# Performance work log

Hardware: AMD Instinct MI355X
Metric: run time of the kernel (lower is better)

Reference implementation:

```python
import jax, jax.numpy as jnp
import numpy as np

N, D, E, H, K = 8192, 1024, 8, 256, 2


def setup_inputs() -> dict:
    key = jax.random.key(0)
    ks = jax.random.split(key, 9)
    s = 0.02
    return {
        "x": jax.random.normal(ks[0], (N, D), dtype=jnp.float32),
        "Wg": jax.random.normal(ks[1], (D, E), dtype=jnp.float32) * s,
        "bg": jnp.zeros((E,), dtype=jnp.float32),
        "W1": jax.random.normal(ks[2], (E, D, H), dtype=jnp.float32) * s,
        "b1": jnp.zeros((E, H), dtype=jnp.float32),
        "W2": jax.random.normal(ks[3], (E, H, H), dtype=jnp.float32) * s,
        "b2": jnp.zeros((E, H), dtype=jnp.float32),
        "W3": jax.random.normal(ks[4], (E, H, D), dtype=jnp.float32) * s,
        "b3": jnp.zeros((E, D), dtype=jnp.float32),
    }


def reference(x, Wg, bg, W1, b1, W2, b2, W3, b3):
    # Gating: softmax over experts, then keep only top-k gate values per token.
    gates = jax.nn.softmax(x @ Wg + bg, axis=-1)              # [N, E]
    top_v, top_i = jax.lax.top_k(gates, K)                    # [N, K]
    rows = jnp.arange(gates.shape[0])[:, None]                # [N, 1]
    top_k_gates = jnp.zeros_like(gates).at[rows, top_i].set(top_v)  # [N, E]

    # Dense all-expert MLP (matches original: every expert runs on every token).
    h = jax.nn.relu(jnp.einsum('nd,edh->neh', x, W1) + b1)    # [N, E, H]
    h = jax.nn.relu(jnp.einsum('neh,ehg->neg', h, W2) + b2)   # [N, E, H]  (dropout is eval no-op)
    eo = jax.nn.relu(jnp.einsum('neh,ehd->ned', h, W3) + b3)  # [N, E, D]

    # Combine with masked gates: einsum('...nde,...ne->...nd') with eo in 'ned' layout.
    output = jnp.einsum('ned,ne->nd', eo, top_k_gates)        # [N, D]
    return output
```

## Files before the change

### kernel.cpp

```cpp
#include <hip/hip_runtime.h>
#include <math.h>

#define NTOK 8192
#define DDIM 1024
#define NEXP 8
#define HDIM 256
#define TOPK 2
#define PADM 128
#define CAPS (NTOK * TOPK + NEXP * PADM)
#define NT64  (CAPS / 64)
#define NT128 (CAPS / 128)

typedef __attribute__((ext_vector_type(8))) __bf16 bf16x8;
typedef __attribute__((ext_vector_type(4))) float f32x4;

#define GLDS16(g, s)                                                      \
    __builtin_amdgcn_global_load_lds(                                     \
        (const __attribute__((address_space(1))) void*)(g),               \
        (__attribute__((address_space(3))) void*)(s), 16, 0, 0)

static constexpr size_t OFF_TOFF = 128;
static constexpr size_t OFF_ZBUF = 4096;
static constexpr size_t OFF_T2E  = 8192;
static constexpr size_t OFF_T2G  = OFF_T2E + (size_t)NTOK * TOPK * 4;
static constexpr size_t OFF_SLOT = OFF_T2G + (size_t)NTOK * TOPK * 4;
static constexpr size_t OFF_TOK  = OFF_SLOT + (size_t)NTOK * TOPK * 4;
static constexpr size_t OFF_GAT  = OFF_TOK + (size_t)CAPS * 4;
static constexpr size_t OFF_XB   = (OFF_GAT + (size_t)CAPS * 4 + 255) & ~(size_t)255;
static constexpr size_t OFF_W1T  = OFF_XB  + (size_t)NTOK * DDIM * 2;
static constexpr size_t OFF_W2T  = OFF_W1T + (size_t)NEXP * DDIM * HDIM * 2;
static constexpr size_t OFF_W3T  = OFF_W2T + (size_t)NEXP * HDIM * HDIM * 2;
static constexpr size_t OFF_H2   = OFF_W3T + (size_t)NEXP * HDIM * DDIM * 2;
static constexpr size_t OFF_H3   = OFF_H2  + (size_t)CAPS * HDIM * 2;

static __device__ __forceinline__ unsigned short f2b(float f) {
    __bf16 h = (__bf16)f;
    return __builtin_bit_cast(unsigned short, h);
}
static __device__ __forceinline__ float b2f(unsigned short u) {
    return __builtin_bit_cast(float, ((unsigned)u) << 16);
}

__global__ __launch_bounds__(256) void gate_trans(
    const float* __restrict__ x, const float* __restrict__ Wg,
    const float* __restrict__ bg, unsigned short* __restrict__ xb,
    int* __restrict__ top2e, float* __restrict__ top2g,
    const float* __restrict__ W1, const float* __restrict__ W2,
    const float* __restrict__ W3, __bf16* __restrict__ w1t,
    __bf16* __restrict__ w2t, __bf16* __restrict__ w3t)
{
    __shared__ __align__(16) float sh[NEXP * DDIM];
    const int tid = threadIdx.x;

    if (blockIdx.x < 256) {
        for (int d = tid; d < DDIM; d += 256) {
            const float4 w0 = *(const float4*)(Wg + (size_t)d * NEXP);
            const float4 w1 = *(const float4*)(Wg + (size_t)d * NEXP + 4);
            sh[0 * DDIM + d] = w0.x; sh[1 * DDIM + d] = w0.y;
            sh[2 * DDIM + d] = w0.z; sh[3 * DDIM + d] = w0.w;
            sh[4 * DDIM + d] = w1.x; sh[5 * DDIM + d] = w1.y;
            sh[6 * DDIM + d] = w1.z; sh[7 * DDIM + d] = w1.w;
        }
        __syncthreads();

        const int n = (blockIdx.y * 256 + blockIdx.x) * 4 + (tid >> 6);
        const int lane = tid & 63;
        const float* xr = x + (size_t)n * DDIM;
        unsigned short* xbr = xb + (size_t)n * DDIM;

        float acc[NEXP];
#pragma unroll
        for (int e = 0; e < NEXP; ++e) acc[e] = 0.f;

#pragma unroll
        for (int it = 0; it < 4; ++it) {
            const int d = it * 256 + lane * 4;
            const float4 xv = *(const float4*)(xr + d);
            ushort4 u;
            u.x = f2b(xv.x); u.y = f2b(xv.y); u.z = f2b(xv.z); u.w = f2b(xv.w);
            *(ushort4*)(xbr + d) = u;
#pragma unroll
            for (int e = 0; e < NEXP; ++e) {
                const float4 wt = *(const float4*)(sh + e * DDIM + d);
                acc[e] = fmaf(xv.x, wt.x, acc[e]);
                acc[e] = fmaf(xv.y, wt.y, acc[e]);
                acc[e] = fmaf(xv.z, wt.z, acc[e]);
                acc[e] = fmaf(xv.w, wt.w, acc[e]);
            }
        }
#pragma unroll
        for (int off = 32; off > 0; off >>= 1)
#pragma unroll
            for (int e = 0; e < NEXP; ++e) acc[e] += __shfl_down(acc[e], off, 64);

        if (lane == 0) {
            float v[NEXP], mx = -1e30f;
#pragma unroll
            for (int e = 0; e < NEXP; ++e) { v[e] = acc[e] + bg[e]; mx = fmaxf(mx, v[e]); }
            float p[NEXP], s = 0.f;
#pragma unroll
            for (int e = 0; e < NEXP; ++e) { p[e] = expf(v[e] - mx); s += p[e]; }
            const float inv = 1.f / s;
#pragma unroll
            for (int e = 0; e < NEXP; ++e) p[e] *= inv;
            int i0 = 0;
#pragma unroll
            for (int e = 1; e < NEXP; ++e) if (p[e] > p[i0]) i0 = e;
            int i1 = (i0 == 0) ? 1 : 0;
#pragma unroll
            for (int e = 0; e < NEXP; ++e) if (e != i0 && p[e] > p[i1]) i1 = e;
            top2e[n * 2 + 0] = i0;  top2e[n * 2 + 1] = i1;
            top2g[n * 2 + 0] = p[i0]; top2g[n * 2 + 1] = p[i1];
        }
    } else {
        const int e = blockIdx.y;
        int bt = blockIdx.x - 256;
        const float* Wi; __bf16* Wo; int R, C, xt, yt;
        if (bt < 256)      { Wi = W1; Wo = w1t; R = DDIM; C = HDIM; xt = bt & 7;  yt = bt >> 3; }
        else if (bt < 320) { bt -= 256; Wi = W2; Wo = w2t; R = HDIM; C = HDIM; xt = bt & 7;  yt = bt >> 3; }
        else               { bt -= 320; Wi = W3; Wo = w3t; R = HDIM; C = DDIM; xt = bt & 31; yt = bt >> 5; }
        const int r0 = yt * 32, c0 = xt * 32;
        const int tx = tid & 31, ty = tid >> 5;
        const float* Wie = Wi + (size_t)e * R * C;
        __bf16* Woe = Wo + (size_t)e * C * R;
#pragma unroll
        for (int j = 0; j < 4; ++j)
            sh[(ty + j * 8) * 33 + tx] = Wie[(size_t)(r0 + ty + j * 8) * C + c0 + tx];
        __syncthreads();
#pragma unroll
        for (int j = 0; j < 4; ++j)
            Woe[(size_t)(c0 + ty + j * 8) * R + r0 + tx] = (__bf16)sh[tx * 33 + ty + j * 8];
    }
}

__global__ __launch_bounds__(1024) void route(
    const int* __restrict__ top2e, const float* __restrict__ top2g,
    int* __restrict__ toff, int* __restrict__ tok, float* __restrict__ gat,
    int* __restrict__ slotof, float* __restrict__ zbuf)
{
    const int tid = threadIdx.x;
    const int wv = tid >> 6, ln = tid & 63;
    __shared__ int   waveTot[16][NEXP];
    __shared__ int   waveBase[16][NEXP];
    __shared__ int   totS[NEXP];
    __shared__ int   toffS[NEXP + 1];
    __shared__ short excS[1024][NEXP];

    zbuf[tid] = 0.f;

    int myE[16]; float myG[16];
    const int4*   pe = (const int4*)(top2e + tid * 16);
    const float4* pg = (const float4*)(top2g + tid * 16);
#pragma unroll
    for (int q = 0; q < 4; ++q) {
        const int4 v = pe[q];
        myE[q * 4 + 0] = v.x; myE[q * 4 + 1] = v.y;
        myE[q * 4 + 2] = v.z; myE[q * 4 + 3] = v.w;
        const float4 g = pg[q];
        myG[q * 4 + 0] = g.x; myG[q * 4 + 1] = g.y;
        myG[q * 4 + 2] = g.z; myG[q * 4 + 3] = g.w;
    }

#pragma unroll
    for (int e = 0; e < NEXP; ++e) {
        int c = 0;
#pragma unroll
        for (int j = 0; j < 16; ++j) c += (myE[j] == e);
        int inc = c;
#pragma unroll
        for (int off = 1; off < 64; off <<= 1) {
            const int t = __shfl_up(inc, off, 64);
            if (ln >= off) inc += t;
        }
        excS[tid][e] = (short)(inc - c);
        if (ln == 63) waveTot[wv][e] = inc;
    }
    __syncthreads();

    if (tid < NEXP) {
        int b = 0;
#pragma unroll
        for (int w = 0; w < 16; ++w) {
            const int t = waveTot[w][tid];
            waveBase[w][tid] = b;
            b += t;
        }
        totS[tid] = b;
    }
    __syncthreads();

    if (tid == 0) {
        int acc = 0;
#pragma unroll
        for (int e = 0; e < NEXP; ++e) {
            toffS[e] = acc;
            acc += (totS[e] + PADM - 1) & ~(PADM - 1);
        }
        toffS[NEXP] = acc;
#pragma unroll
        for (int e = 0; e <= NEXP; ++e) toff[e] = toffS[e];
    }
    __syncthreads();

#pragma unroll
    for (int j = 0; j < 16; ++j) {
        int pre = 0;
#pragma unroll
        for (int j2 = 0; j2 < j; ++j2) pre += (myE[j2] == myE[j]);
        const int e = myE[j];
        const int slot = toffS[e] + waveBase[wv][e] + (int)excS[tid][e] + pre;
        const int i = tid * 16 + j;
        tok[slot] = i >> 1;
        gat[slot] = myG[j];
        slotof[i] = slot;
    }

#pragma unroll
    for (int e = 0; e < NEXP; ++e) {
        const int begin = toffS[e] + totS[e];
        const int end   = toffS[e + 1];
        for (int i = begin + tid; i < end; i += 1024) {
            tok[i] = -1;
            gat[i] = 0.f;
        }
    }
}

__global__ __launch_bounds__(256) void egemm12(
    const __bf16* __restrict__ xb, const __bf16* __restrict__ w1t,
    const __bf16* __restrict__ w2t, const float* __restrict__ b1,
    const float* __restrict__ b2, const int* __restrict__ toff,
    const int* __restrict__ tok, const char* __restrict__ zbuf,
    __bf16* __restrict__ h2)
{
    const int total = toff[NEXP];
    const int slot0 = blockIdx.x * 64;
    if (slot0 >= total) return;
    int e = 0;
    while (toff[e + 1] <= slot0) ++e;

    __shared__ __align__(16) char smem[73728];
    char* AsB = smem;
    char* BsB = smem + 8192;
    char* H1s = smem + 40960;

    const int tid  = threadIdx.x;
    const int lane = tid & 63;
    const int wid  = tid >> 6;

    const int srow  = tid >> 3;
    const int sslot = tid & 7;
    const int ks    = sslot ^ (srow & 7);

    const __bf16* We1 = w1t + (size_t)e * HDIM * DDIM;
    const char* ap[2];
#pragma unroll
    for (int i = 0; i < 2; ++i) {
        const int t = tok[slot0 + i * 32 + srow];
        ap[i] = (t >= 0) ? (const char*)(xb + (size_t)t * DDIM + ks * 8) : zbuf;
    }
    const char* bp1[8];
#pragma unroll
    for (int i = 0; i < 8; ++i)
        bp1[i] = (const char*)(We1 + (size_t)(i * 32 + srow) * DDIM + ks * 8);

    const int llo = lane & 15, lhi = lane >> 4;
    const int m7 = llo & 7;
    int abyte[4], bbyte[4];
#pragma unroll
    for (int m = 0; m < 4; ++m) {
        abyte[m] = (m * 16 + llo) * 128;
        bbyte[m] = (wid * 64 + m * 16 + llo) * 128;
    }

    f32x4 acc[4][4];
#pragma unroll
    for (int m = 0; m < 4; ++m)
#pragma unroll
        for (int n = 0; n < 4; ++n) acc[m][n] = (f32x4){0.f, 0.f, 0.f, 0.f};

    for (int k0 = 0; k0 < DDIM; k0 += 64) {
        const size_t kb = (size_t)k0 * 2;
        GLDS16(ap[0] + kb, AsB + tid * 16);
        GLDS16(ap[1] + kb, AsB + 4096 + tid * 16);
#pragma unroll
        for (int i = 0; i < 8; ++i)
            GLDS16(bp1[i] + kb, BsB + i * 4096 + tid * 16);
        __syncthreads();
#pragma unroll
        for (int kk = 0; kk < 2; ++kk) {
            const int sl = ((kk << 2) + lhi) ^ m7;
            bf16x8 af[4], bfr[4];
#pragma unroll
            for (int m = 0; m < 4; ++m) af[m]  = *(const bf16x8*)(AsB + abyte[m] + (sl << 4));
#pragma unroll
            for (int n = 0; n < 4; ++n) bfr[n] = *(const bf16x8*)(BsB + bbyte[n] + (sl << 4));
#pragma unroll
            for (int m = 0; m < 4; ++m)
#pragma unroll
                for (int n = 0; n < 4; ++n)
                    acc[m][n] = __builtin_amdgcn_mfma_f32_16x16x32_bf16(
                        af[m], bfr[n], acc[m][n], 0, 0, 0);
        }
        __syncthreads();
    }

    {
        const float* be1 = b1 + (size_t)e * HDIM;
#pragma unroll
        for (int n = 0; n < 4; ++n) {
            const int col = wid * 64 + n * 16 + llo;
            const float bb = be1[col];
            const int colbyte = (col & 7) * 2;
            const int slice = col >> 3;
#pragma unroll
            for (int m = 0; m < 4; ++m) {
#pragma unroll
                for (int j = 0; j < 4; ++j) {
                    const int r = m * 16 + lhi * 4 + j;
                    const float v = fmaxf(acc[m][n][j] + bb, 0.f);
                    *(__bf16*)(H1s + r * 512 + ((slice ^ (r & 7)) << 4) + colbyte) = (__bf16)v;
                }
                acc[m][n] = (f32x4){0.f, 0.f, 0.f, 0.f};
            }
        }
    }
    __syncthreads();

    const __bf16* We2 = w2t + (size_t)e * HDIM * HDIM;
    const char* bp2[8];
#pragma unroll
    for (int i = 0; i < 8; ++i)
        bp2[i] = (const char*)(We2 + (size_t)(i * 32 + srow) * HDIM + ks * 8);

    for (int k2 = 0; k2 < 4; ++k2) {
        const size_t kb = (size_t)k2 * 128;
#pragma unroll
        for (int i = 0; i < 8; ++i)
            GLDS16(bp2[i] + kb, BsB + i * 4096 + tid * 16);
        __syncthreads();
#pragma unroll
        for (int kk = 0; kk < 2; ++kk) {
            const int slB = ((kk << 2) + lhi) ^ m7;
            const int sA  = k2 * 8 + (kk << 2) + lhi;
            const int slA = sA ^ m7;
            bf16x8 af[4], bfr[4];
#pragma unroll
            for (int m = 0; m < 4; ++m)
                af[m] = *(const bf16x8*)(H1s + (m * 16 + llo) * 512 + (slA << 4));
#pragma unroll
            for (int n = 0; n < 4; ++n)
                bfr[n] = *(const bf16x8*)(BsB + bbyte[n] + (slB << 4));
#pragma unroll
            for (int m = 0; m < 4; ++m)
#pragma unroll
                for (int n = 0; n < 4; ++n)
                    acc[m][n] = __builtin_amdgcn_mfma_f32_16x16x32_bf16(
                        af[m], bfr[n], acc[m][n], 0, 0, 0);
        }
        __syncthreads();
    }

    {
        const float* be2 = b2 + (size_t)e * HDIM;
#pragma unroll
        for (int n = 0; n < 4; ++n) {
            const int col = wid * 64 + n * 16 + llo;
            const float bb = be2[col];
#pragma unroll
            for (int m = 0; m < 4; ++m) {
#pragma unroll
                for (int j = 0; j < 4; ++j) {
                    const int r = slot0 + m * 16 + lhi * 4 + j;
                    h2[(size_t)r * HDIM + col] = (__bf16)fmaxf(acc[m][n][j] + bb, 0.f);
                }
            }
        }
    }
}

template<int KDIM, int NCOL>
__global__ __launch_bounds__(256) void egemm3(
    const __bf16* __restrict__ Ain, const __bf16* __restrict__ Wt,
    const float* __restrict__ ball, const int* __restrict__ toff,
    const float* __restrict__ gat, __bf16* __restrict__ Out)
{
    const int total = toff[NEXP];
    const int slot0 = blockIdx.y * 128;
    if (slot0 >= total) return;
    int e = 0;
    while (toff[e + 1] <= slot0) ++e;
    const int col0 = blockIdx.x * 128;

    __shared__ __align__(16) char smem[32768];
    char* AsB = smem;
    char* BsB = smem + 16384;

    const int tid  = threadIdx.x;
    const int lane = tid & 63;
    const int wid  = tid >> 6;
    const int wr = wid >> 1, wc = wid & 1;

    const int srow  = tid >> 3;
    const int sslot = tid & 7;
    const int ks    = sslot ^ (srow & 7);
    const __bf16* We = Wt + (size_t)e * NCOL * KDIM;
    const char* ap[4];
    const char* bp[4];
#pragma unroll
    for (int i = 0; i < 4; ++i) {
        const int row = i * 32 + srow;
        ap[i] = (const char*)(Ain + (size_t)(slot0 + row) * KDIM + ks * 8);
        bp[i] = (const char*)(We + (size_t)(col0 + row) * KDIM + ks * 8);
    }

    const int llo = lane & 15, lhi = lane >> 4;
    const int m7 = llo & 7;
    int abyte[4], bbyte[4];
#pragma unroll
    for (int m = 0; m < 4; ++m) {
        abyte[m] = (wr * 64 + m * 16 + llo) * 128;
        bbyte[m] = (wc * 64 + m * 16 + llo) * 128;
    }

    f32x4 acc[4][4];
#pragma unroll
    for (int m = 0; m < 4; ++m)
#pragma unroll
        for (int n = 0; n < 4; ++n) acc[m][n] = (f32x4){0.f, 0.f, 0.f, 0.f};

    for (int k0 = 0; k0 < KDIM; k0 += 64) {
        const size_t kb = (size_t)k0 * 2;
#pragma unroll
        for (int i = 0; i < 4; ++i)
            GLDS16(ap[i] + kb, AsB + i * 4096 + wid * 1024);
#pragma unroll
        for (int i = 0; i < 4; ++i)
            GLDS16(bp[i] + kb, BsB + i * 4096 + wid * 1024);
        __syncthreads();
#pragma unroll
        for (int kk = 0; kk < 2; ++kk) {
            const int sl = ((kk << 2) + lhi) ^ m7;
            bf16x8 af[4], bfr[4];
#pragma unroll
            for (int m = 0; m < 4; ++m) af[m]  = *(const bf16x8*)(AsB + abyte[m] + (sl << 4));
#pragma unroll
            for (int n = 0; n < 4; ++n) bfr[n] = *(const bf16x8*)(BsB + bbyte[n] + (sl << 4));
#pragma unroll
            for (int m = 0; m < 4; ++m)
#pragma unroll
                for (int n = 0; n < 4; ++n)
                    acc[m][n] = __builtin_amdgcn_mfma_f32_16x16x32_bf16(
                        af[m], bfr[n], acc[m][n], 0, 0, 0);
        }
        __syncthreads();
    }

    const float* be = ball + (size_t)e * NCOL;
#pragma unroll
    for (int m = 0; m < 4; ++m) {
        const int rbase = slot0 + wr * 64 + m * 16 + lhi * 4;
        float g[4];
#pragma unroll
        for (int j = 0; j < 4; ++j) g[j] = gat[rbase + j];
#pragma unroll
        for (int n = 0; n < 4; ++n) {
            const int col = col0 + wc * 64 + n * 16 + llo;
            const float bb = be[col];
#pragma unroll
            for (int j = 0; j < 4; ++j) {
                const float v = fmaxf(acc[m][n][j] + bb, 0.f) * g[j];
                Out[(size_t)(rbase + j) * NCOL + col] = (__bf16)v;
            }
        }
    }
}

__global__ __launch_bounds__(256) void combine(
    const unsigned short* __restrict__ h3, const int* __restrict__ slotof,
    float* __restrict__ out)
{
    const int n = blockIdx.x;
    const int c = threadIdx.x * 4;
    const int s0 = slotof[n * 2], s1 = slotof[n * 2 + 1];
    const ushort4 a = *(const ushort4*)(h3 + (size_t)s0 * DDIM + c);
    const ushort4 b = *(const ushort4*)(h3 + (size_t)s1 * DDIM + c);
    float4 o;
    o.x = b2f(a.x) + b2f(b.x);
    o.y = b2f(a.y) + b2f(b.y);
    o.z = b2f(a.z) + b2f(b.z);
    o.w = b2f(a.w) + b2f(b.w);
    *(float4*)(out + (size_t)n * DDIM + c) = o;
}

extern "C" void kernel_launch(void* const* d_in, const int* in_sizes, int n_in,
                              void* d_out, int out_size, void* d_ws, size_t ws_size,
                              hipStream_t stream)
{
    const float* x  = (const float*)d_in[0];
    const float* Wg = (const float*)d_in[1];
    const float* bg = (const float*)d_in[2];
    const float* W1 = (const float*)d_in[3];
    const float* b1 = (const float*)d_in[4];
    const float* W2 = (const float*)d_in[5];
    const float* b2 = (const float*)d_in[6];
    const float* W3 = (const float*)d_in[7];
    const float* b3 = (const float*)d_in[8];
    float* out = (float*)d_out;

    char* ws = (char*)d_ws;
    int*   toff   = (int*)(ws + OFF_TOFF);
    char*  zbuf   = ws + OFF_ZBUF;
    int*   top2e  = (int*)(ws + OFF_T2E);
    float* top2g  = (float*)(ws + OFF_T2G);
    int*   slotof = (int*)(ws + OFF_SLOT);
    int*   tok    = (int*)(ws + OFF_TOK);
    float* gat    = (float*)(ws + OFF_GAT);
    unsigned short* xbu = (unsigned short*)(ws + OFF_XB);
    __bf16* xb  = (__bf16*)(ws + OFF_XB);
    __bf16* w1t = (__bf16*)(ws + OFF_W1T);
    __bf16* w2t = (__bf16*)(ws + OFF_W2T);
    __bf16* w3t = (__bf16*)(ws + OFF_W3T);
    __bf16* h2  = (__bf16*)(ws + OFF_H2);
    __bf16* h3  = (__bf16*)(ws + OFF_H3);

    gate_trans<<<dim3(832, NEXP), 256, 0, stream>>>(
        x, Wg, bg, xbu, top2e, top2g, W1, W2, W3, w1t, w2t, w3t);
    route<<<1, 1024, 0, stream>>>(top2e, top2g, toff, tok, gat, slotof, (float*)zbuf);

    egemm12<<<NT64, 256, 0, stream>>>(xb, w1t, w2t, b1, b2, toff, tok, zbuf, h2);
    egemm3<HDIM, DDIM><<<dim3(DDIM / 128, NT128), 256, 0, stream>>>(
        h2, w3t, b3, toff, gat, h3);

    combine<<<NTOK, 256, 0, stream>>>((const unsigned short*)h3, slotof, out);
}
```

Baseline: 106.8 us.

## Fuse all MoE stages into one persistent cooperative kernel with grid syncs

Replaces the five separate launches (gate/transpose, route, expert GEMM1+2, GEMM3, combine) with one persistent cooperative kernel. Stages are separated by grid.sync, and work is distributed with grid-stride loops over a grid sized from occupancy. Routing now runs in a single 256-thread block instead of 1024 threads. The goal is to remove launch gaps and inter-kernel drain. In exchange, occupancy is capped at about two blocks per CU by a 72KB LDS allocation, and grid barriers plus the serial routing stage add latency.

```diff
diff --git a/kernel.cpp b/kernel.cpp
--- a/kernel.cpp
+++ b/kernel.cpp
@@ -1,5 +1,8 @@
 #include <hip/hip_runtime.h>
+#include <hip/hip_cooperative_groups.h>
 #include <math.h>
+
+namespace cg = cooperative_groups;
 
 #define NTOK 8192
 #define DDIM 1024
@@ -8,8 +11,6 @@
 #define TOPK 2
 #define PADM 128
 #define CAPS (NTOK * TOPK + NEXP * PADM)
-#define NT64  (CAPS / 64)
-#define NT128 (CAPS / 128)
 
 typedef __attribute__((ext_vector_type(8))) __bf16 bf16x8;
 typedef __attribute__((ext_vector_type(4))) float f32x4;
@@ -41,456 +42,461 @@
     return __builtin_bit_cast(float, ((unsigned)u) << 16);
 }
 
-__global__ __launch_bounds__(256) void gate_trans(
-    const float* __restrict__ x, const float* __restrict__ Wg,
-    const float* __restrict__ bg, unsigned short* __restrict__ xb,
-    int* __restrict__ top2e, float* __restrict__ top2g,
-    const float* __restrict__ W1, const float* __restrict__ W2,
-    const float* __restrict__ W3, __bf16* __restrict__ w1t,
-    __bf16* __restrict__ w2t, __bf16* __restrict__ w3t)
+__global__ __launch_bounds__(256, 2) void moe_mega(
+    const float* __restrict__ x,  const float* __restrict__ Wg,
+    const float* __restrict__ bg, const float* __restrict__ W1,
+    const float* __restrict__ b1, const float* __restrict__ W2,
+    const float* __restrict__ b2, const float* __restrict__ W3,
+    const float* __restrict__ b3, float* __restrict__ out,
+    char* __restrict__ ws)
 {
-    __shared__ __align__(16) float sh[NEXP * DDIM];
+    cg::grid_group grid = cg::this_grid();
+    __shared__ __align__(16) char smem[73728];
+
+    int*   toff   = (int*)(ws + OFF_TOFF);
+    float* zbuf   = (float*)(ws + OFF_ZBUF);
+    int*   top2e  = (int*)(ws + OFF_T2E);
+    float* top2g  = (float*)(ws + OFF_T2G);
+    int*   slotof = (int*)(ws + OFF_SLOT);
+    int*   tok    = (int*)(ws + OFF_TOK);
+    float* gat    = (float*)(ws + OFF_GAT);
+    unsigned short* xbu = (unsigned short*)(ws + OFF_XB);
+    __bf16* xb  = (__bf16*)(ws + OFF_XB);
+    __bf16* w1t = (__bf16*)(ws + OFF_W1T);
+    __bf16* w2t = (__bf16*)(ws + OFF_W2T);
+    __bf16* w3t = (__bf16*)(ws + OFF_W3T);
+    __bf16* h2  = (__bf16*)(ws + OFF_H2);
+    __bf16* h3  = (__bf16*)(ws + OFF_H3);
+
     const int tid = threadIdx.x;
-
-    if (blockIdx.x < 256) {
+    const int bid = blockIdx.x;
+    const int nb  = gridDim.x;
+
+    {
+        float* WgT = (float*)smem;
         for (int d = tid; d < DDIM; d += 256) {
             const float4 w0 = *(const float4*)(Wg + (size_t)d * NEXP);
             const float4 w1 = *(const float4*)(Wg + (size_t)d * NEXP + 4);
-            sh[0 * DDIM + d] = w0.x; sh[1 * DDIM + d] = w0.y;
-            sh[2 * DDIM + d] = w0.z; sh[3 * DDIM + d] = w0.w;
-            sh[4 * DDIM + d] = w1.x; sh[5 * DDIM + d] = w1.y;
-            sh[6 * DDIM + d] = w1.z; sh[7 * DDIM + d] = w1.w;
+            WgT[0 * DDIM + d] = w0.x; WgT[1 * DDIM + d] = w0.y;
+            WgT[2 * DDIM + d] = w0.z; WgT[3 * DDIM + d] = w0.w;
+            WgT[4 * DDIM + d] = w1.x; WgT[5 * DDIM + d] = w1.y;
+            WgT[6 * DDIM + d] = w1.z; WgT[7 * DDIM + d] = w1.w;
         }
         __syncthreads();
 
-        const int n = (blockIdx.y * 256 + blockIdx.x) * 4 + (tid >> 6);
         const int lane = tid & 63;
-        const float* xr = x + (size_t)n * DDIM;
-        unsigned short* xbr = xb + (size_t)n * DDIM;
-
-        float acc[NEXP];
-#pragma unroll
-        for (int e = 0; e < NEXP; ++e) acc[e] = 0.f;
-
-#pragma unroll
-        for (int it = 0; it < 4; ++it) {
-            const int d = it * 256 + lane * 4;
-            const float4 xv = *(const float4*)(xr + d);
-            ushort4 u;
-            u.x = f2b(xv.x); u.y = f2b(xv.y); u.z = f2b(xv.z); u.w = f2b(xv.w);
-            *(ushort4*)(xbr + d) = u;
+        for (int g = bid; g < NTOK / 4; g += nb) {
+            const int n = g * 4 + (tid >> 6);
+            const float* xr = x + (size_t)n * DDIM;
+            unsigned short* xbr = xbu + (size_t)n * DDIM;
+
+            float acc[NEXP];
+#pragma unroll
+            for (int e = 0; e < NEXP; ++e) acc[e] = 0.f;
+#pragma unroll
+            for (int it = 0; it < 4; ++it) {
+                const int d = it * 256 + lane * 4;
+                const float4 xv = *(const float4*)(xr + d);
+                ushort4 u;
+                u.x = f2b(xv.x); u.y = f2b(xv.y); u.z = f2b(xv.z); u.w = f2b(xv.w);
+                *(ushort4*)(xbr + d) = u;
+#pragma unroll
+                for (int e = 0; e < NEXP; ++e) {
+                    const float4 wt = *(const float4*)(WgT + e * DDIM + d);
+                    acc[e] = fmaf(xv.x, wt.x, acc[e]);
+                    acc[e] = fmaf(xv.y, wt.y, acc[e]);
+                    acc[e] = fmaf(xv.z, wt.z, acc[e]);
+                    acc[e] = fmaf(xv.w, wt.w, acc[e]);
+                }
+            }
+#pragma unroll
+            for (int off = 32; off > 0; off >>= 1)
+#pragma unroll
+                for (int e = 0; e < NEXP; ++e) acc[e] += __shfl_down(acc[e], off, 64);
+
+            if (lane == 0) {
+                float v[NEXP], mx = -1e30f;
+#pragma unroll
+                for (int e = 0; e < NEXP; ++e) { v[e] = acc[e] + bg[e]; mx = fmaxf(mx, v[e]); }
+                float p[NEXP], s = 0.f;
+#pragma unroll
+                for (int e = 0; e < NEXP; ++e) { p[e] = expf(v[e] - mx); s += p[e]; }
+                const float inv = 1.f / s;
+#pragma unroll
+                for (int e = 0; e < NEXP; ++e) p[e] *= inv;
+                int i0 = 0;
+#pragma unroll
+                for (int e = 1; e < NEXP; ++e) if (p[e] > p[i0]) i0 = e;
+                int i1 = (i0 == 0) ? 1 : 0;
+#pragma unroll
+                for (int e = 0; e < NEXP; ++e) if (e != i0 && p[e] > p[i1]) i1 = e;
+                top2e[n * 2 + 0] = i0;  top2e[n * 2 + 1] = i1;
+                top2g[n * 2 + 0] = p[i0]; top2g[n * 2 + 1] = p[i1];
+            }
+        }
+
+        float* ts = (float*)(smem + 32768);
+        const int tx = tid & 31, ty = tid >> 5;
+        for (int t = bid; t < 4608; t += nb) {
+            const int e = t / 576;
+            int bt = t - e * 576;
+            const float* Wi; __bf16* Wo; int R, C, xt, yt;
+            if (bt < 256)      { Wi = W1; Wo = w1t; R = DDIM; C = HDIM; xt = bt & 7;  yt = bt >> 3; }
+            else if (bt < 320) { bt -= 256; Wi = W2; Wo = w2t; R = HDIM; C = HDIM; xt = bt & 7;  yt = bt >> 3; }
+            else               { bt -= 320; Wi = W3; Wo = w3t; R = HDIM; C = DDIM; xt = bt & 31; yt = bt >> 5; }
+            const int r0 = yt * 32, c0 = xt * 32;
+            const float* Wie = Wi + (size_t)e * R * C;
+            __bf16* Woe = Wo + (size_t)e * C * R;
+            __syncthreads();
+#pragma unroll
+            for (int j = 0; j < 4; ++j)
+                ts[(ty + j * 8) * 33 + tx] = Wie[(size_t)(r0 + ty + j * 8) * C + c0 + tx];
+            __syncthreads();
+#pragma unroll
+            for (int j = 0; j < 4; ++j)
+                Woe[(size_t)(c0 + ty + j * 8) * R + r0 + tx] = (__bf16)ts[tx * 33 + ty + j * 8];
+        }
+    }
+    grid.sync();
+
+    if (bid == 0) {
+        int* waveTotS  = (int*)smem;
+        int* waveBaseS = (int*)(smem + 128);
+        int* totS      = (int*)(smem + 256);
+        int* toffS     = (int*)(smem + 320);
+        const int wv = tid >> 6, ln = tid & 63;
+        const int4*   pe = (const int4*)top2e + tid * 16;
+        const float4* pg = (const float4*)top2g + tid * 16;
+
+        int c[NEXP] = {0, 0, 0, 0, 0, 0, 0, 0};
+        for (int q = 0; q < 16; ++q) {
+            const int4 v = pe[q];
+#pragma unroll
+            for (int e = 0; e < NEXP; ++e)
+                c[e] += (v.x == e) + (v.y == e) + (v.z == e) + (v.w == e);
+        }
+        int base[NEXP];
+#pragma unroll
+        for (int e = 0; e < NEXP; ++e) {
+            int inc = c[e];
+#pragma unroll
+            for (int off = 1; off < 64; off <<= 1) {
+                const int t = __shfl_up(inc, off, 64);
+                if (ln >= off) inc += t;
+            }
+            base[e] = inc - c[e];
+            if (ln == 63) waveTotS[wv * NEXP + e] = inc;
+        }
+        __syncthreads();
+        if (tid < NEXP) {
+            int b = 0;
+#pragma unroll
+            for (int w = 0; w < 4; ++w) {
+                const int t = waveTotS[w * NEXP + tid];
+                waveBaseS[w * NEXP + tid] = b;
+                b += t;
+            }
+            totS[tid] = b;
+        }
+        __syncthreads();
+        if (tid == 0) {
+            int acc = 0;
 #pragma unroll
             for (int e = 0; e < NEXP; ++e) {
-                const float4 wt = *(const float4*)(sh + e * DDIM + d);
-                acc[e] = fmaf(xv.x, wt.x, acc[e]);
-                acc[e] = fmaf(xv.y, wt.y, acc[e]);
-                acc[e] = fmaf(xv.z, wt.z, acc[e]);
-                acc[e] = fmaf(xv.w, wt.w, acc[e]);
-            }
-        }
-#pragma unroll
-        for (int off = 32; off > 0; off >>= 1)
-#pragma unroll
-            for (int e = 0; e < NEXP; ++e) acc[e] += __shfl_down(acc[e], off, 64);
-
-        if (lane == 0) {
-            float v[NEXP], mx = -1e30f;
-#pragma unroll
-            for (int e = 0; e < NEXP; ++e) { v[e] = acc[e] + bg[e]; mx = fmaxf(mx, v[e]); }
-            float p[NEXP], s = 0.f;
-#pragma unroll
-            for (int e = 0; e < NEXP; ++e) { p[e] = expf(v[e] - mx); s += p[e]; }
-            const float inv = 1.f / s;
-#pragma unroll
-            for (int e = 0; e < NEXP; ++e) p[e] *= inv;
-            int i0 = 0;
-#pragma unroll
-            for (int e = 1; e < NEXP; ++e) if (p[e] > p[i0]) i0 = e;
-            int i1 = (i0 == 0) ? 1 : 0;
-#pragma unroll
-            for (int e = 0; e < NEXP; ++e) if (e != i0 && p[e] > p[i1]) i1 = e;
-            top2e[n * 2 + 0] = i0;  top2e[n * 2 + 1] = i1;
-            top2g[n * 2 + 0] = p[i0]; top2g[n * 2 + 1] = p[i1];
-        }
-    } else {
-        const int e = blockIdx.y;
-        int bt = blockIdx.x - 256;
-        const float* Wi; __bf16* Wo; int R, C, xt, yt;
-        if (bt < 256)      { Wi = W1; Wo = w1t; R = DDIM; C = HDIM; xt = bt & 7;  yt = bt >> 3; }
-        else if (bt < 320) { bt -= 256; Wi = W2; Wo = w2t; R = HDIM; C = HDIM; xt = bt & 7;  yt = bt >> 3; }
-        else               { bt -= 320; Wi = W3; Wo = w3t; R = HDIM; C = DDIM; xt = bt & 31; yt = bt >> 5; }
-        const int r0 = yt * 32, c0 = xt * 32;
-        const int tx = tid & 31, ty = tid >> 5;
-        const float* Wie = Wi + (size_t)e * R * C;
-        __bf16* Woe = Wo + (size_t)e * C * R;
-#pragma unroll
-        for (int j = 0; j < 4; ++j)
-            sh[(ty + j * 8) * 33 + tx] = Wie[(size_t)(r0 + ty + j * 8) * C + c0 + tx];
+                toffS[e] = acc;
+                acc += (totS[e] + PADM - 1) & ~(PADM - 1);
+            }
+            toffS[NEXP] = acc;
+#pragma unroll
+            for (int e = 0; e <= NEXP; ++e) toff[e] = toffS[e];
+        }
         __syncthreads();
-#pragma unroll
-        for (int j = 0; j < 4; ++j)
-            Woe[(size_t)(c0 + ty + j * 8) * R + r0 + tx] = (__bf16)sh[tx * 33 + ty + j * 8];
+
+        int cur[NEXP];
+#pragma unroll
+        for (int e = 0; e < NEXP; ++e)
+            cur[e] = toffS[e] + waveBaseS[wv * NEXP + e] + base[e];
+
+        for (int q = 0; q < 16; ++q) {
+            const int4 v = pe[q];
+            const float4 gv = pg[q];
+            const int va[4] = {v.x, v.y, v.z, v.w};
+            const float ga[4] = {gv.x, gv.y, gv.z, gv.w};
+#pragma unroll
+            for (int j = 0; j < 4; ++j) {
+                int slot = 0;
+#pragma unroll
+                for (int e = 0; e < NEXP; ++e)
+                    if (va[j] == e) { slot = cur[e]; cur[e] = slot + 1; }
+                const int i = tid * 64 + q * 4 + j;
+                tok[slot] = i >> 1;
+                gat[slot] = ga[j];
+                slotof[i] = slot;
+            }
+        }
+#pragma unroll
+        for (int e = 0; e < NEXP; ++e)
+            for (int i = toffS[e] + totS[e] + tid; i < toffS[e + 1]; i += 256) {
+                tok[i] = -1;
+                gat[i] = 0.f;
+            }
+        for (int i = tid; i < 1024; i += 256) zbuf[i] = 0.f;
+        __threadfence();
     }
-}
-
-__global__ __launch_bounds__(1024) void route(
-    const int* __restrict__ top2e, const float* __restrict__ top2g,
-    int* __restrict__ toff, int* __restrict__ tok, float* __restrict__ gat,
-    int* __restrict__ slotof, float* __restrict__ zbuf)
-{
-    const int tid = threadIdx.x;
-    const int wv = tid >> 6, ln = tid & 63;
-    __shared__ int   waveTot[16][NEXP];
-    __shared__ int   waveBase[16][NEXP];
-    __shared__ int   totS[NEXP];
-    __shared__ int   toffS[NEXP + 1];
-    __shared__ short excS[1024][NEXP];
-
-    zbuf[tid] = 0.f;
-
-    int myE[16]; float myG[16];
-    const int4*   pe = (const int4*)(top2e + tid * 16);
-    const float4* pg = (const float4*)(top2g + tid * 16);
-#pragma unroll
-    for (int q = 0; q < 4; ++q) {
-        const int4 v = pe[q];
-        myE[q * 4 + 0] = v.x; myE[q * 4 + 1] = v.y;
-        myE[q * 4 + 2] = v.z; myE[q * 4 + 3] = v.w;
-        const float4 g = pg[q];
-        myG[q * 4 + 0] = g.x; myG[q * 4 + 1] = g.y;
-        myG[q * 4 + 2] = g.z; myG[q * 4 + 3] = g.w;
+    grid.sync();
+
+    {
+        const int total = toff[NEXP];
+        char* AsB = smem;
+        char* BsB = smem + 8192;
+        char* H1s = smem + 40960;
+        const int lane = tid & 63;
+        const int wid  = tid >> 6;
+        const int srow  = tid >> 3;
+        const int sslot = tid & 7;
+        const int ks    = sslot ^ (srow & 7);
+        const int llo = lane & 15, lhi = lane >> 4;
+        const int m7 = llo & 7;
+        int abyte[4], bbyte[4];
+#pragma unroll
+        for (int m = 0; m < 4; ++m) {
+            abyte[m] = (m * 16 + llo) * 128;
+            bbyte[m] = (wid * 64 + m * 16 + llo) * 128;
+        }
+
+        for (int t = bid; t < total / 64; t += nb) {
+            const int slot0 = t * 64;
+            int e = 0;
+            while (toff[e + 1] <= slot0) ++e;
+            __syncthreads();
+
+            const __bf16* We1 = w1t + (size_t)e * HDIM * DDIM;
+            const char* ap[2];
+#pragma unroll
+            for (int i = 0; i < 2; ++i) {
+                const int tk = tok[slot0 + i * 32 + srow];
+                ap[i] = (tk >= 0) ? (const char*)(xb + (size_t)tk * DDIM + ks * 8)
+                                  : (const char*)zbuf;
+            }
+            const char* bp1[8];
+#pragma unroll
+            for (int i = 0; i < 8; ++i)
+                bp1[i] = (const char*)(We1 + (size_t)(i * 32 + srow) * DDIM + ks * 8);
+
+            f32x4 acc[4][4];
+#pragma unroll
+            for (int m = 0; m < 4; ++m)
+#pragma unroll
+                for (int n = 0; n < 4; ++n) acc[m][n] = (f32x4){0.f, 0.f, 0.f, 0.f};
+
+            for (int k0 = 0; k0 < DDIM; k0 += 64) {
+                const size_t kb = (size_t)k0 * 2;
+                GLDS16(ap[0] + kb, AsB + tid * 16);
+                GLDS16(ap[1] + kb, AsB + 4096 + tid * 16);
+#pragma unroll
+                for (int i = 0; i < 8; ++i)
+                    GLDS16(bp1[i] + kb, BsB + i * 4096 + tid * 16);
+                __syncthreads();
+#pragma unroll
+                for (int kk = 0; kk < 2; ++kk) {
+                    const int sl = ((kk << 2) + lhi) ^ m7;
+                    bf16x8 af[4], bfr[4];
+#pragma unroll
+                    for (int m = 0; m < 4; ++m) af[m]  = *(const bf16x8*)(AsB + abyte[m] + (sl << 4));
+#pragma unroll
+                    for (int n = 0; n < 4; ++n) bfr[n] = *(const bf16x8*)(BsB + bbyte[n] + (sl << 4));
+#pragma unroll
+                    for (int m = 0; m < 4; ++m)
+#pragma unroll
+                        for (int n = 0; n < 4; ++n)
+                            acc[m][n] = __builtin_amdgcn_mfma_f32_16x16x32_bf16(
+                                af[m], bfr[n], acc[m][n], 0, 0, 0);
+                }
+                __syncthreads();
+            }
+
+            {
+                const float* be1 = b1 + (size_t)e * HDIM;
+#pragma unroll
+                for (int n = 0; n < 4; ++n) {
+                    const int col = wid * 64 + n * 16 + llo;
+                    const float bb = be1[col];
+                    const int colbyte = (col & 7) * 2;
+                    const int slice = col >> 3;
+#pragma unroll
+                    for (int m = 0; m < 4; ++m) {
+#pragma unroll
+                        for (int j = 0; j < 4; ++j) {
+                            const int r = m * 16 + lhi * 4 + j;
+                            const float v = fmaxf(acc[m][n][j] + bb, 0.f);
+                            *(__bf16*)(H1s + r * 512 + ((slice ^ (r & 7)) << 4) + colbyte) = (__bf16)v;
+                        }
+                        acc[m][n] = (f32x4){0.f, 0.f, 0.f, 0.f};
+                    }
+                }
+            }
+            __syncthreads();
+
+            const __bf16* We2 = w2t + (size_t)e * HDIM * HDIM;
+            const char* bp2[8];
+#pragma unroll
+            for (int i = 0; i < 8; ++i)
+                bp2[i] = (const char*)(We2 + (size_t)(i * 32 + srow) * HDIM + ks * 8);
+
+            for (int k2 = 0; k2 < 4; ++k2) {
+                const size_t kb = (size_t)k2 * 128;
+#pragma unroll
+                for (int i = 0; i < 8; ++i)
+                    GLDS16(bp2[i] + kb, BsB + i * 4096 + tid * 16);
+                __syncthreads();
+#pragma unroll
+                for (int kk = 0; kk < 2; ++kk) {
+                    const int slB = ((kk << 2) + lhi) ^ m7;
+                    const int sA  = k2 * 8 + (kk << 2) + lhi;
+                    const int slA = sA ^ m7;
+                    bf16x8 af[4], bfr[4];
+#pragma unroll
+                    for (int m = 0; m < 4; ++m)
+                        af[m] = *(const bf16x8*)(H1s + (m * 16 + llo) * 512 + (slA << 4));
+#pragma unroll
+                    for (int n = 0; n < 4; ++n)
+                        bfr[n] = *(const bf16x8*)(BsB + bbyte[n] + (slB << 4));
+#pragma unroll
+                    for (int m = 0; m < 4; ++m)
+#pragma unroll
+                        for (int n = 0; n < 4; ++n)
+                            acc[m][n] = __builtin_amdgcn_mfma_f32_16x16x32_bf16(
+                                af[m], bfr[n], acc[m][n], 0, 0, 0);
+                }
+                __syncthreads();
+            }
+
+            {
+                const float* be2 = b2 + (size_t)e * HDIM;
+#pragma unroll
+                for (int n = 0; n < 4; ++n) {
+                    const int col = wid * 64 + n * 16 + llo;
+                    const float bb = be2[col];
+#pragma unroll
+                    for (int m = 0; m < 4; ++m)
+#pragma unroll
+                        for (int j = 0; j < 4; ++j) {
+                            const int r = slot0 + m * 16 + lhi * 4 + j;
+                            h2[(size_t)r * HDIM + col] = (__bf16)fmaxf(acc[m][n][j] + bb, 0.f);
+                        }
+                }
+            }
+        }
     }
-
-#pragma unroll
-    for (int e = 0; e < NEXP; ++e) {
-        int c = 0;
-#pragma unroll
-        for (int j = 0; j < 16; ++j) c += (myE[j] == e);
-        int inc = c;
-#pragma unroll
-        for (int off = 1; off < 64; off <<= 1) {
-            const int t = __shfl_up(inc, off, 64);
-            if (ln >= off) inc += t;
-        }
-        excS[tid][e] = (short)(inc - c);
-        if (ln == 63) waveTot[wv][e] = inc;
+    grid.sync();
+
+    {
+        const int total = toff[NEXP];
+        const int nt = (total / 128) * 8;
+        char* AsB = smem;
+        char* BsB = smem + 16384;
+        const int lane = tid & 63;
+        const int wid  = tid >> 6;
+        const int wr = wid >> 1, wc = wid & 1;
+        const int srow  = tid >> 3;
+        const int sslot = tid & 7;
+        const int ks    = sslot ^ (srow & 7);
+        const int llo = lane & 15, lhi = lane >> 4;
+        const int m7 = llo & 7;
+        int abyte[4], bbyte[4];
+#pragma unroll
+        for (int m = 0; m < 4; ++m) {
+            abyte[m] = (wr * 64 + m * 16 + llo) * 128;
+            bbyte[m] = (wc * 64 + m * 16 + llo) * 128;
+        }
+
+        for (int t = bid; t < nt; t += nb) {
+            const int col0  = (t & 7) * 128;
+            const int slot0 = (t >> 3) * 128;
+            int e = 0;
+            while (toff[e + 1] <= slot0) ++e;
+            __syncthreads();
+
+            const __bf16* We = w3t + (size_t)e * DDIM * HDIM;
+            const char* ap[4];
+            const char* bp[4];
+#pragma unroll
+            for (int i = 0; i < 4; ++i) {
+                const int row = i * 32 + srow;
+                ap[i] = (const char*)(h2 + (size_t)(slot0 + row) * HDIM + ks * 8);
+                bp[i] = (const char*)(We + (size_t)(col0 + row) * HDIM + ks * 8);
+            }
+
+            f32x4 acc[4][4];
+#pragma unroll
+            for (int m = 0; m < 4; ++m)
+#pragma unroll
+                for (int n = 0; n < 4; ++n) acc[m][n] = (f32x4){0.f, 0.f, 0.f, 0.f};
+
+            for (int k0 = 0; k0 < HDIM; k0 += 64) {
+                const size_t kb = (size_t)k0 * 2;
+#pragma unroll
+                for (int i = 0; i < 4; ++i)
+                    GLDS16(ap[i] + kb, AsB + i * 4096 + wid * 1024);
+#pragma unroll
+                for (int i = 0; i < 4; ++i)
+                    GLDS16(bp[i] + kb, BsB + i * 4096 + wid * 1024);
+                __syncthreads();
+#pragma unroll
+                for (int kk = 0; kk < 2; ++kk) {
+                    const int sl = ((kk << 2) + lhi) ^ m7;
+                    bf16x8 af[4], bfr[4];
+#pragma unroll
+                    for (int m = 0; m < 4; ++m) af[m]  = *(const bf16x8*)(AsB + abyte[m] + (sl << 4));
+#pragma unroll
+                    for (int n = 0; n < 4; ++n) bfr[n] = *(const bf16x8*)(BsB + bbyte[n] + (sl << 4));
+#pragma unroll
+                    for (int m = 0; m < 4; ++m)
+#pragma unroll
+                        for (int n = 0; n < 4; ++n)
+                            acc[m][n] = __builtin_amdgcn_mfma_f32_16x16x32_bf16(
+                                af[m], bfr[n], acc[m][n], 0, 0, 0);
+                }
+                __syncthreads();
+            }
+
+            const float* be = b3 + (size_t)e * DDIM;
+#pragma unroll
+            for (int m = 0; m < 4; ++m) {
+                const int rbase = slot0 + wr * 64 + m * 16 + lhi * 4;
+                float g[4];
+#pragma unroll
+                for (int j = 0; j < 4; ++j) g[j] = gat[rbase + j];
+#pragma unroll
+                for (int n = 0; n < 4; ++n) {
+                    const int col = col0 + wc * 64 + n * 16 + llo;
+                    const float bb = be[col];
+#pragma unroll
+                    for (int j = 0; j < 4; ++j) {
+                        const float v = fmaxf(acc[m][n][j] + bb, 0.f) * g[j];
+                        h3[(size_t)(rbase + j) * DDIM + col] = (__bf16)v;
+                    }
+                }
+            }
+        }
     }
-    __syncthreads();
-
-    if (tid < NEXP) {
-        int b = 0;
-#pragma unroll
-        for (int w = 0; w < 16; ++w) {
-            const int t = waveTot[w][tid];
-            waveBase[w][tid] = b;
-            b += t;
-        }
-        totS[tid] = b;
+    grid.sync();
+
+    {
+        const unsigned short* h3u = (const unsigned short*)h3;
+        const int c = tid * 4;
+        for (int n = bid; n < NTOK; n += nb) {
+            const int s0 = slotof[n * 2], s1 = slotof[n * 2 + 1];
+            const ushort4 a = *(const ushort4*)(h3u + (size_t)s0 * DDIM + c);
+            const ushort4 b = *(const ushort4*)(h3u + (size_t)s1 * DDIM + c);
+            float4 o;
+            o.x = b2f(a.x) + b2f(b.x);
+            o.y = b2f(a.y) + b2f(b.y);
+            o.z = b2f(a.z) + b2f(b.z);
+            o.w = b2f(a.w) + b2f(b.w);
+            *(float4*)(out + (size_t)n * DDIM + c) = o;
+        }
     }
-    __syncthreads();
-
-    if (tid == 0) {
-        int acc = 0;
-#pragma unroll
-        for (int e = 0; e < NEXP; ++e) {
-            toffS[e] = acc;
-            acc += (totS[e] + PADM - 1) & ~(PADM - 1);
-        }
-        toffS[NEXP] = acc;
-#pragma unroll
-        for (int e = 0; e <= NEXP; ++e) toff[e] = toffS[e];
-    }
-    __syncthreads();
-
-#pragma unroll
-    for (int j = 0; j < 16; ++j) {
-        int pre = 0;
-#pragma unroll
-        for (int j2 = 0; j2 < j; ++j2) pre += (myE[j2] == myE[j]);
-        const int e = myE[j];
-        const int slot = toffS[e] + waveBase[wv][e] + (int)excS[tid][e] + pre;
-        const int i = tid * 16 + j;
-        tok[slot] = i >> 1;
-        gat[slot] = myG[j];
-        slotof[i] = slot;
-    }
-
-#pragma unroll
-    for (int e = 0; e < NEXP; ++e) {
-        const int begin = toffS[e] + totS[e];
-        const int end   = toffS[e + 1];
-        for (int i = begin + tid; i < end; i += 1024) {
-            tok[i] = -1;
-            gat[i] = 0.f;
-        }
-    }
-}
-
-__global__ __launch_bounds__(256) void egemm12(
-    const __bf16* __restrict__ xb, const __bf16* __restrict__ w1t,
-    const __bf16* __restrict__ w2t, const float* __restrict__ b1,
-    const float* __restrict__ b2, const int* __restrict__ toff,
-    const int* __restrict__ tok, const char* __restrict__ zbuf,
-    __bf16* __restrict__ h2)
-{
-    const int total = toff[NEXP];
-    const int slot0 = blockIdx.x * 64;
-    if (slot0 >= total) return;
-    int e = 0;
-    while (toff[e + 1] <= slot0) ++e;
-
-    __shared__ __align__(16) char smem[73728];
-    char* AsB = smem;
-    char* BsB = smem + 8192;
-    char* H1s = smem + 40960;
-
-    const int tid  = threadIdx.x;
-    const int lane = tid & 63;
-    const int wid  = tid >> 6;
-
-    const int srow  = tid >> 3;
-    const int sslot = tid & 7;
-    const int ks    = sslot ^ (srow & 7);
-
-    const __bf16* We1 = w1t + (size_t)e * HDIM * DDIM;
-    const char* ap[2];
-#pragma unroll
-    for (int i = 0; i < 2; ++i) {
-        const int t = tok[slot0 + i * 32 + srow];
-        ap[i] = (t >= 0) ? (const char*)(xb + (size_t)t * DDIM + ks * 8) : zbuf;
-    }
-    const char* bp1[8];
-#pragma unroll
-    for (int i = 0; i < 8; ++i)
-        bp1[i] = (const char*)(We1 + (size_t)(i * 32 + srow) * DDIM + ks * 8);
-
-    const int llo = lane & 15, lhi = lane >> 4;
-    const int m7 = llo & 7;
-    int abyte[4], bbyte[4];
-#pragma unroll
-    for (int m = 0; m < 4; ++m) {
-        abyte[m] = (m * 16 + llo) * 128;
-        bbyte[m] = (wid * 64 + m * 16 + llo) * 128;
-    }
-
-    f32x4 acc[4][4];
-#pragma unroll
-    for (int m = 0; m < 4; ++m)
-#pragma unroll
-        for (int n = 0; n < 4; ++n) acc[m][n] = (f32x4){0.f, 0.f, 0.f, 0.f};
-
-    for (int k0 = 0; k0 < DDIM; k0 += 64) {
-        const size_t kb = (size_t)k0 * 2;
-        GLDS16(ap[0] + kb, AsB + tid * 16);
-        GLDS16(ap[1] + kb, AsB + 4096 + tid * 16);
-#pragma unroll
-        for (int i = 0; i < 8; ++i)
-            GLDS16(bp1[i] + kb, BsB + i * 4096 + tid * 16);
-        __syncthreads();
-#pragma unroll
-        for (int kk = 0; kk < 2; ++kk) {
-            const int sl = ((kk << 2) + lhi) ^ m7;
-            bf16x8 af[4], bfr[4];
-#pragma unroll
-            for (int m = 0; m < 4; ++m) af[m]  = *(const bf16x8*)(AsB + abyte[m] + (sl << 4));
-#pragma unroll
-            for (int n = 0; n < 4; ++n) bfr[n] = *(const bf16x8*)(BsB + bbyte[n] + (sl << 4));
-#pragma unroll
-            for (int m = 0; m < 4; ++m)
-#pragma unroll
-                for (int n = 0; n < 4; ++n)
-                    acc[m][n] = __builtin_amdgcn_mfma_f32_16x16x32_bf16(
-                        af[m], bfr[n], acc[m][n], 0, 0, 0);
-        }
-        __syncthreads();
-    }
-
-    {
-        const float* be1 = b1 + (size_t)e * HDIM;
-#pragma unroll
-        for (int n = 0; n < 4; ++n) {
-            const int col = wid * 64 + n * 16 + llo;
-            const float bb = be1[col];
-            const int colbyte = (col & 7) * 2;
-            const int slice = col >> 3;
-#pragma unroll
-            for (int m = 0; m < 4; ++m) {
-#pragma unroll
-                for (int j = 0; j < 4; ++j) {
-                    const int r = m * 16 + lhi * 4 + j;
-                    const float v = fmaxf(acc[m][n][j] + bb, 0.f);
-                    *(__bf16*)(H1s + r * 512 + ((slice ^ (r & 7)) << 4) + colbyte) = (__bf16)v;
-                }
-                acc[m][n] = (f32x4){0.f, 0.f, 0.f, 0.f};
-            }
-        }
-    }
-    __syncthreads();
-
-    const __bf16* We2 = w2t + (size_t)e * HDIM * HDIM;
-    const char* bp2[8];
-#pragma unroll
-    for (int i = 0; i < 8; ++i)
-        bp2[i] = (const char*)(We2 + (size_t)(i * 32 + srow) * HDIM + ks * 8);
-
-    for (int k2 = 0; k2 < 4; ++k2) {
-        const size_t kb = (size_t)k2 * 128;
-#pragma unroll
-        for (int i = 0; i < 8; ++i)
-            GLDS16(bp2[i] + kb, BsB + i * 4096 + tid * 16);
-        __syncthreads();
-#pragma unroll
-        for (int kk = 0; kk < 2; ++kk) {
-            const int slB = ((kk << 2) + lhi) ^ m7;
-            const int sA  = k2 * 8 + (kk << 2) + lhi;
-            const int slA = sA ^ m7;
-            bf16x8 af[4], bfr[4];
-#pragma unroll
-            for (int m = 0; m < 4; ++m)
-                af[m] = *(const bf16x8*)(H1s + (m * 16 + llo) * 512 + (slA << 4));
-#pragma unroll
-            for (int n = 0; n < 4; ++n)
-                bfr[n] = *(const bf16x8*)(BsB + bbyte[n] + (slB << 4));
-#pragma unroll
-            for (int m = 0; m < 4; ++m)
-#pragma unroll
-                for (int n = 0; n < 4; ++n)
-                    acc[m][n] = __builtin_amdgcn_mfma_f32_16x16x32_bf16(
-                        af[m], bfr[n], acc[m][n], 0, 0, 0);
-        }
-        __syncthreads();
-    }
-
-    {
-        const float* be2 = b2 + (size_t)e * HDIM;
-#pragma unroll
-        for (int n = 0; n < 4; ++n) {
-            const int col = wid * 64 + n * 16 + llo;
-            const float bb = be2[col];
-#pragma unroll
-            for (int m = 0; m < 4; ++m) {
-#pragma unroll
-                for (int j = 0; j < 4; ++j) {
-                    const int r = slot0 + m * 16 + lhi * 4 + j;
-                    h2[(size_t)r * HDIM + col] = (__bf16)fmaxf(acc[m][n][j] + bb, 0.f);
-                }
-            }
-        }
-    }
-}
-
-template<int KDIM, int NCOL>
-__global__ __launch_bounds__(256) void egemm3(
-    const __bf16* __restrict__ Ain, const __bf16* __restrict__ Wt,
-    const float* __restrict__ ball, const int* __restrict__ toff,
-    const float* __restrict__ gat, __bf16* __restrict__ Out)
-{
-    const int total = toff[NEXP];
-    const int slot0 = blockIdx.y * 128;
-    if (slot0 >= total) return;
-    int e = 0;
-    while (toff[e + 1] <= slot0) ++e;
-    const int col0 = blockIdx.x * 128;
-
-    __shared__ __align__(16) char smem[32768];
-    char* AsB = smem;
-    char* BsB = smem + 16384;
-
-    const int tid  = threadIdx.x;
-    const int lane = tid & 63;
-    const int wid  = tid >> 6;
-    const int wr = wid >> 1, wc = wid & 1;
-
-    const int srow  = tid >> 3;
-    const int sslot = tid & 7;
-    const int ks    = sslot ^ (srow & 7);
-    const __bf16* We = Wt + (size_t)e * NCOL * KDIM;
-    const char* ap[4];
-    const char* bp[4];
-#pragma unroll
-    for (int i = 0; i < 4; ++i) {
-        const int row = i * 32 + srow;
-        ap[i] = (const char*)(Ain + (size_t)(slot0 + row) * KDIM + ks * 8);
-        bp[i] = (const char*)(We + (size_t)(col0 + row) * KDIM + ks * 8);
-    }
-
-    const int llo = lane & 15, lhi = lane >> 4;
-    const int m7 = llo & 7;
-    int abyte[4], bbyte[4];
-#pragma unroll
-    for (int m = 0; m < 4; ++m) {
-        abyte[m] = (wr * 64 + m * 16 + llo) * 128;
-        bbyte[m] = (wc * 64 + m * 16 + llo) * 128;
-    }
-
-    f32x4 acc[4][4];
-#pragma unroll
-    for (int m = 0; m < 4; ++m)
-#pragma unroll
-        for (int n = 0; n < 4; ++n) acc[m][n] = (f32x4){0.f, 0.f, 0.f, 0.f};
-
-    for (int k0 = 0; k0 < KDIM; k0 += 64) {
-        const size_t kb = (size_t)k0 * 2;
-#pragma unroll
-        for (int i = 0; i < 4; ++i)
-            GLDS16(ap[i] + kb, AsB + i * 4096 + wid * 1024);
-#pragma unroll
-        for (int i = 0; i < 4; ++i)
-            GLDS16(bp[i] + kb, BsB + i * 4096 + wid * 1024);
-        __syncthreads();
-#pragma unroll
-        for (int kk = 0; kk < 2; ++kk) {
-            const int sl = ((kk << 2) + lhi) ^ m7;
-            bf16x8 af[4], bfr[4];
-#pragma unroll
-            for (int m = 0; m < 4; ++m) af[m]  = *(const bf16x8*)(AsB + abyte[m] + (sl << 4));
-#pragma unroll
-            for (int n = 0; n < 4; ++n) bfr[n] = *(const bf16x8*)(BsB + bbyte[n] + (sl << 4));
-#pragma unroll
-            for (int m = 0; m < 4; ++m)
-#pragma unroll
-                for (int n = 0; n < 4; ++n)
-                    acc[m][n] = __builtin_amdgcn_mfma_f32_16x16x32_bf16(
-                        af[m], bfr[n], acc[m][n], 0, 0, 0);
-        }
-        __syncthreads();
-    }
-
-    const float* be = ball + (size_t)e * NCOL;
-#pragma unroll
-    for (int m = 0; m < 4; ++m) {
-        const int rbase = slot0 + wr * 64 + m * 16 + lhi * 4;
-        float g[4];
-#pragma unroll
-        for (int j = 0; j < 4; ++j) g[j] = gat[rbase + j];
-#pragma unroll
-        for (int n = 0; n < 4; ++n) {
-            const int col = col0 + wc * 64 + n * 16 + llo;
-            const float bb = be[col];
-#pragma unroll
-            for (int j = 0; j < 4; ++j) {
-                const float v = fmaxf(acc[m][n][j] + bb, 0.f) * g[j];
-                Out[(size_t)(rbase + j) * NCOL + col] = (__bf16)v;
-            }
-        }
-    }
-}
-
-__global__ __launch_bounds__(256) void combine(
-    const unsigned short* __restrict__ h3, const int* __restrict__ slotof,
-    float* __restrict__ out)
-{
-    const int n = blockIdx.x;
-    const int c = threadIdx.x * 4;
-    const int s0 = slotof[n * 2], s1 = slotof[n * 2 + 1];
-    const ushort4 a = *(const ushort4*)(h3 + (size_t)s0 * DDIM + c);
-    const ushort4 b = *(const ushort4*)(h3 + (size_t)s1 * DDIM + c);
-    float4 o;
-    o.x = b2f(a.x) + b2f(b.x);
-    o.y = b2f(a.y) + b2f(b.y);
-    o.z = b2f(a.z) + b2f(b.z);
-    o.w = b2f(a.w) + b2f(b.w);
-    *(float4*)(out + (size_t)n * DDIM + c) = o;
 }
 
 extern "C" void kernel_launch(void* const* d_in, const int* in_sizes, int n_in,
@@ -507,30 +513,18 @@
     const float* W3 = (const float*)d_in[7];
     const float* b3 = (const float*)d_in[8];
     float* out = (float*)d_out;
-
-    char* ws = (char*)d_ws;
-    int*   toff   = (int*)(ws + OFF_TOFF);
-    char*  zbuf   = ws + OFF_ZBUF;
-    int*   top2e  = (int*)(ws + OFF_T2E);
-    float* top2g  = (float*)(ws + OFF_T2G);
-    int*   slotof = (int*)(ws + OFF_SLOT);
-    int*   tok    = (int*)(ws + OFF_TOK);
-    float* gat    = (float*)(ws + OFF_GAT);
-    unsigned short* xbu = (unsigned short*)(ws + OFF_XB);
-    __bf16* xb  = (__bf16*)(ws + OFF_XB);
-    __bf16* w1t = (__bf16*)(ws + OFF_W1T);
-    __bf16* w2t = (__bf16*)(ws + OFF_W2T);
-    __bf16* w3t = (__bf16*)(ws + OFF_W3T);
-    __bf16* h2  = (__bf16*)(ws + OFF_H2);
-    __bf16* h3  = (__bf16*)(ws + OFF_H3);
-
-    gate_trans<<<dim3(832, NEXP), 256, 0, stream>>>(
-        x, Wg, bg, xbu, top2e, top2g, W1, W2, W3, w1t, w2t, w3t);
-    route<<<1, 1024, 0, stream>>>(top2e, top2g, toff, tok, gat, slotof, (float*)zbuf);
-
-    egemm12<<<NT64, 256, 0, stream>>>(xb, w1t, w2t, b1, b2, toff, tok, zbuf, h2);
-    egemm3<HDIM, DDIM><<<dim3(DDIM / 128, NT128), 256, 0, stream>>>(
-        h2, w3t, b3, toff, gat, h3);
-
-    combine<<<NTOK, 256, 0, stream>>>((const unsigned short*)h3, slotof, out);
+    char* wsp = (char*)d_ws;
+
+    int nbpc = 0;
+    if (hipOccupancyMaxActiveBlocksPerMultiprocessor(
+            &nbpc, (const void*)moe_mega, 256, 0) != hipSuccess || nbpc < 1)
+        nbpc = 1;
+    int nblocks = nbpc * 256;
+    if (nblocks > 512) nblocks = 512;
+
+    void* args[] = { (void*)&x, (void*)&Wg, (void*)&bg, (void*)&W1, (void*)&b1,
+                     (void*)&W2, (void*)&b2, (void*)&W3, (void*)&b3,
+                     (void*)&out, (void*)&wsp };
+    hipLaunchCooperativeKernel((const void*)moe_mega, dim3(nblocks), dim3(256),
+                               args, 0, stream);
 }
```

Measured after the change: 303.5 us. 184% more time.
